# Kernel optimization log

Hardware: AMD Instinct MI355X
Metric: run time of the kernel (lower is better)

## Reference

```python
import jax, jax.numpy as jnp
import numpy as np

B, T, C, H = 4, 2048, 1024, 16
D = C // H  # head dim = 64

def setup_inputs() -> dict:
    key = jax.random.key(0)
    k1, k2, k3 = jax.random.split(key, 3)
    x = jax.random.normal(k1, (B, T, C), dtype=jnp.float32)
    w_attn = jax.random.normal(k2, (C, 3 * C), dtype=jnp.float32) * 0.02
    b_attn = jnp.zeros((3 * C,), dtype=jnp.float32)
    w_proj = jax.random.normal(k3, (C, C), dtype=jnp.float32) * 0.02
    b_proj = jnp.zeros((C,), dtype=jnp.float32)
    return {"x": x, "w_attn": w_attn, "b_attn": b_attn, "w_proj": w_proj, "b_proj": b_proj}

def reference(x, w_attn, b_attn, w_proj, b_proj):
    Bx, Tx, Cx = x.shape
    qkv = x @ w_attn + b_attn  # [B, T, 3C]
    q, k, v = jnp.split(qkv, 3, axis=2)
    # [B, H, T, D]
    q = q.reshape(Bx, Tx, H, D).swapaxes(1, 2)
    k = k.reshape(Bx, Tx, H, D).swapaxes(1, 2)
    v = v.reshape(Bx, Tx, H, D).swapaxes(1, 2)
    scale = 1.0 / jnp.sqrt(jnp.asarray(D, dtype=x.dtype))
    att = jnp.einsum('bhqd,bhkd->bhqk', q, k) * scale  # [B, H, T, T]
    causal = jnp.tril(jnp.ones((Tx, Tx), dtype=bool))
    att = jnp.where(causal[None, None], att, -jnp.inf)
    att = jax.nn.softmax(att, axis=-1)
    y = jnp.einsum('bhqk,bhkd->bhqd', att, v)  # [B, H, T, D]
    y = y.swapaxes(1, 2).reshape(Bx, Tx, Cx)
    return y @ w_proj + b_proj
```

## Files before the change

kernel.cpp:

```cpp
#include <hip/hip_runtime.h>
#include <hip/hip_bf16.h>
#include <cstdint>

#define B_ 4
#define T_ 2048
#define C_ 1024
#define H_ 16
#define D_ 64

#define BM 128
#define BN 128
#define BK 64
#define NT (C_ / BK)

typedef __bf16 bf16x8 __attribute__((ext_vector_type(8)));
typedef float f32x4 __attribute__((ext_vector_type(4)));

static __device__ __forceinline__ unsigned short f2bf(float f) {
    unsigned int i = __float_as_uint(f);
    unsigned int r = (i + 0x7FFFu + ((i >> 16) & 1u)) >> 16;
    return (unsigned short)r;
}
static __device__ __forceinline__ float exp2_fast(float x) {
    float r;
    asm("v_exp_f32 %0, %1" : "=v"(r) : "v"(x));
    return r;
}

static __device__ __forceinline__ void gl_lds16(const unsigned short* g,
                                                unsigned short* l) {
    __builtin_amdgcn_global_load_lds(
        (const __attribute__((address_space(1))) unsigned int*)g,
        (__attribute__((address_space(3))) unsigned int*)l, 16, 0, 0);
}

__global__ __launch_bounds__(256)
void convert_f32_bf16(const float* __restrict__ in,
                      unsigned short* __restrict__ out, int n) {
    int i = (blockIdx.x * 256 + threadIdx.x) * 8;
    if (i < n) {
        float4 a = *(const float4*)(in + i);
        float4 b = *(const float4*)(in + i + 4);
        ushort4 s0 = {f2bf(a.x), f2bf(a.y), f2bf(a.z), f2bf(a.w)};
        ushort4 s1 = {f2bf(b.x), f2bf(b.y), f2bf(b.z), f2bf(b.w)};
        *(ushort4*)(out + i) = s0;
        *(ushort4*)(out + i + 4) = s1;
    }
}

__global__ void transpose_f32_bf16(const float* __restrict__ in,
                                   unsigned short* __restrict__ out,
                                   int R, int Cc) {
    __shared__ unsigned short tile[32][33];
    int c0 = blockIdx.x * 32;
    int r0 = blockIdx.y * 32;
    int tx = threadIdx.x, ty = threadIdx.y;
    #pragma unroll
    for (int i = ty; i < 32; i += 8)
        tile[i][tx] = f2bf(in[(size_t)(r0 + i) * Cc + c0 + tx]);
    __syncthreads();
    #pragma unroll
    for (int i = ty; i < 32; i += 8)
        out[(size_t)(c0 + i) * R + r0 + tx] = tile[tx][i];
}

#define GEMM128_CORE(APTR, ASTRIDE, BTPTR)                                    \
    int tid = threadIdx.x;                                                    \
    int nwg = gridDim.x * gridDim.y;                                          \
    int flat = blockIdx.y * gridDim.x + blockIdx.x;                           \
    int swz = (flat & 7) * (nwg >> 3) + (flat >> 3);                          \
    int bx = swz % gridDim.x;                                                 \
    int by = swz / gridDim.x;                                                 \
    int row0 = by * BM;                                                       \
    int col0 = bx * BN;                                                       \
    int wave = tid >> 6, lane = tid & 63;                                     \
    int wm = wave >> 1, wn = wave & 1;                                        \
    int m16 = lane & 15, quad = lane >> 4;                                    \
    int srow = tid >> 3;                                                      \
    int scs = ((tid & 7) ^ (srow & 7)) * 8;                                   \
    const unsigned short* aps = (APTR) + (size_t)(row0 + srow) * (ASTRIDE)    \
                                + scs;                                        \
    const unsigned short* bps = (BTPTR) + (size_t)(col0 + srow) * C_ + scs;   \
    f32x4 acc[4][4];                                                          \
    _Pragma("unroll")                                                         \
    for (int i = 0; i < 4; ++i)                                               \
    _Pragma("unroll")                                                         \
    for (int j = 0; j < 4; ++j)                                               \
        acc[i][j] = (f32x4){0.f, 0.f, 0.f, 0.f};                              \
    auto STAGE = [&](int t, int buf) {                                        \
        int koff = t * BK;                                                    \
        unsigned short* ad = smem + buf * 8192 + tid * 8;                     \
        unsigned short* bd = smem + 16384 + buf * 8192 + tid * 8;             \
        _Pragma("unroll")                                                     \
        for (int l = 0; l < 4; ++l) {                                         \
            gl_lds16(aps + (size_t)(l * 32) * (ASTRIDE) + koff, ad + l * 2048);\
            gl_lds16(bps + (size_t)(l * 32) * C_ + koff, bd + l * 2048);      \
        }                                                                     \
    };                                                                        \
    int rbA = wm * 64 + m16;                                                  \
    int rbB = wn * 64 + m16;                                                  \
    int pc0 = ((0 + quad) ^ (m16 & 7)) * 8;                                   \
    int pc1 = ((4 + quad) ^ (m16 & 7)) * 8;                                   \
    STAGE(0, 0);                                                              \
    asm volatile("s_waitcnt vmcnt(0)" ::: "memory");                          \
    __builtin_amdgcn_s_barrier();                                             \
    for (int t = 0; t < NT; ++t) {                                            \
        int buf = t & 1;                                                      \
        if (t + 1 < NT) STAGE(t + 1, buf ^ 1);                                \
        const unsigned short* Abuf = smem + buf * 8192;                       \
        const unsigned short* Bbuf = smem + 16384 + buf * 8192;               \
        bf16x8 a0[4], a1[4], b0[4], b1[4];                                    \
        _Pragma("unroll")                                                     \
        for (int i = 0; i < 4; ++i) {                                         \
            a0[i] = *(const bf16x8*)(Abuf + (rbA + i * 16) * 64 + pc0);       \
            a1[i] = *(const bf16x8*)(Abuf + (rbA + i * 16) * 64 + pc1);       \
        }                                                                     \
        _Pragma("unroll")                                                     \
        for (int j = 0; j < 4; ++j) {                                         \
            b0[j] = *(const bf16x8*)(Bbuf + (rbB + j * 16) * 64 + pc0);       \
            b1[j] = *(const bf16x8*)(Bbuf + (rbB + j * 16) * 64 + pc1);       \
        }                                                                     \
        __builtin_amdgcn_s_setprio(1);                                        \
        _Pragma("unroll")                                                     \
        for (int i = 0; i < 4; ++i)                                           \
        _Pragma("unroll")                                                     \
        for (int j = 0; j < 4; ++j) {                                         \
            acc[i][j] = __builtin_amdgcn_mfma_f32_16x16x32_bf16(              \
                a0[i], b0[j], acc[i][j], 0, 0, 0);                            \
            acc[i][j] = __builtin_amdgcn_mfma_f32_16x16x32_bf16(              \
                a1[i], b1[j], acc[i][j], 0, 0, 0);                            \
        }                                                                     \
        __builtin_amdgcn_s_setprio(0);                                        \
        asm volatile("s_waitcnt vmcnt(0)" ::: "memory");                      \
        __builtin_amdgcn_s_barrier();                                        \
    }                                                                         \
    __syncthreads();

__global__ __launch_bounds__(256, 2)
void gemm_qkv(const unsigned short* __restrict__ A,
              const unsigned short* __restrict__ Bt,
              const float* __restrict__ bias,
              unsigned short* __restrict__ qkv,
              unsigned short* __restrict__ vt,
              int M, float qscale) {
    __shared__ __align__(16) unsigned short smem[32768];
    GEMM128_CORE(A, C_, Bt)

    float bv[4];
    #pragma unroll
    for (int j = 0; j < 4; ++j)
        bv[j] = bias[col0 + wn * 64 + j * 16 + m16];

    unsigned short* wbuf = smem + wave * 2048;
    bool isV = (col0 >= 2 * C_);
    float sc = (col0 < C_) ? qscale : 1.0f;
    int b_loc = row0 >> 11;
    int trow0 = (row0 & 2047) + wm * 64;
    int head = isV ? ((col0 - 2 * C_ + wn * 64) >> 6) : 0;
    unsigned short* vtb = vt + (size_t)((b_loc * H_ + head) * 64) * T_;

    #pragma unroll
    for (int sub = 0; sub < 4; ++sub) {
        int i0 = (sub >> 1) << 1;
        int j0 = (sub & 1) << 1;
        #pragma unroll
        for (int jj = 0; jj < 2; ++jj) {
            #pragma unroll
            for (int ii = 0; ii < 2; ++ii) {
                #pragma unroll
                for (int rr = 0; rr < 4; ++rr) {
                    int rl = ii * 16 + quad * 4 + rr;
                    int cl = jj * 16 + m16;
                    unsigned short hv =
                        f2bf((acc[i0 + ii][j0 + jj][rr] + bv[j0 + jj]) * sc);
                    if (!isV) wbuf[rl * 40 + cl] = hv;
                    else      wbuf[cl * 40 + rl] = hv;
                }
            }
        }
        __builtin_amdgcn_sched_barrier(0);
        if (!isV) {
            #pragma unroll
            for (int it = 0; it < 4; ++it) {
                int rl = it * 8 + (lane >> 3);
                int cc = (lane & 7) << 2;
                uint2 v2 = *(const uint2*)&wbuf[rl * 40 + cc];
                int rowg = row0 + wm * 64 + i0 * 16 + rl;
                int colg = col0 + wn * 64 + j0 * 16 + cc;
                *(uint2*)&qkv[(size_t)rowg * (2 * C_) + colg] = v2;
            }
        } else {
            #pragma unroll
            for (int it = 0; it < 4; ++it) {
                int dsub = it * 8 + (lane >> 3);
                int tc = (lane & 7) << 2;
                uint2 v2 = *(const uint2*)&wbuf[dsub * 40 + tc];
                int d = j0 * 16 + dsub;
                int tg = trow0 + i0 * 16 + tc;
                *(uint2*)&vtb[(size_t)d * T_ + tg] = v2;
            }
        }
        __builtin_amdgcn_sched_barrier(0);
    }
}

__global__ __launch_bounds__(256, 2)
void gemm_out(const unsigned short* __restrict__ A,
              const unsigned short* __restrict__ Bt,
              const float* __restrict__ bias,
              float* __restrict__ Cmat,
              int M) {
    const int N = C_;
    __shared__ __align__(16) unsigned short smem[32768];
    GEMM128_CORE(A, (2 * C_), Bt)

    #pragma unroll
    for (int j = 0; j < 4; ++j) {
        int col = col0 + wn * 64 + j * 16 + m16;
        float bvv = bias[col];
        #pragma unroll
        for (int i = 0; i < 4; ++i) {
            int row = row0 + wm * 64 + i * 16 + quad * 4;
            #pragma unroll
            for (int rr = 0; rr < 4; ++rr)
                Cmat[(size_t)(row + rr) * N + col] = acc[i][j][rr] + bvv;
        }
    }
}

__global__ __launch_bounds__(256)
void attn_mfma(unsigned short* __restrict__ qkv,
               const unsigned short* __restrict__ vt) {
    __shared__ __align__(16) unsigned short Ks[2][64][64];
    __shared__ __align__(16) unsigned short Vs[2][64][64];
    __shared__ __align__(16) unsigned short Pb[4][16][72];

    int bh = blockIdx.x;
    int b = bh >> 4, h = bh & 15;
    int qb = (T_ / 64 - 1) - blockIdx.y;
    int tid = threadIdx.x;
    int wave = tid >> 6;
    int lane = tid & 63;
    int m16 = lane & 15, quad = lane >> 4;

    const size_t rs = 2 * C_;
    unsigned short* base = qkv + (size_t)b * T_ * rs + h * 64;
    const unsigned short* kb0 = base + C_;
    const unsigned short* vtb = vt + (size_t)bh * 64 * T_;

    int qrow = qb * 64 + wave * 16 + m16;
    const unsigned short* qp = base + (size_t)qrow * rs;
    bf16x8 qf0 = *(const bf16x8*)(qp + quad * 8);
    bf16x8 qf1 = *(const bf16x8*)(qp + 32 + quad * 8);

    f32x4 o[4];
    #pragma unroll
    for (int dt = 0; dt < 4; ++dt) o[dt] = (f32x4){0.f, 0.f, 0.f, 0.f};
    float lrow[4] = {0.f, 0.f, 0.f, 0.f};

    int qg0 = qb * 64 + wave * 16 + quad * 4;
    int ntiles = qb + 1;

    int srow = tid >> 3;
    int schs = ((tid & 7) ^ (srow & 7)) * 8;
    const unsigned short* kps = kb0 + (size_t)srow * rs + schs;
    const unsigned short* vps = vtb + (size_t)srow * T_ + schs;
    unsigned short* kdst = &Ks[0][0][0] + wave * 512;
    unsigned short* vdst = &Vs[0][0][0] + wave * 512;

    auto STAGE = [&](int kt, int buf) {
        const unsigned short* ks = kps + (size_t)(kt * 64) * rs;
        const unsigned short* vs = vps + kt * 64;
        unsigned short* kd = kdst + buf * 4096;
        unsigned short* vd = vdst + buf * 4096;
        gl_lds16(ks, kd);
        gl_lds16(ks + (size_t)32 * rs, kd + 2048);
        gl_lds16(vs, vd);
        gl_lds16(vs + (size_t)32 * T_, vd + 2048);
    };

    int kpc0 = ((0 + quad) ^ (m16 & 7)) << 3;
    int kpc1 = ((4 + quad) ^ (m16 & 7)) << 3;

    STAGE(0, 0);
    asm volatile("s_waitcnt vmcnt(0)" ::: "memory");
    __builtin_amdgcn_s_barrier();

    for (int kt = 0; kt < ntiles; ++kt) {
        int cur = kt & 1;
        if (kt + 1 < ntiles) STAGE(kt + 1, cur ^ 1);

        f32x4 s[4];
        #pragma unroll
        for (int st = 0; st < 4; ++st) {
            f32x4 acc = (f32x4){0.f, 0.f, 0.f, 0.f};
            bf16x8 k0 = *(const bf16x8*)&Ks[cur][st * 16 + m16][kpc0];
            bf16x8 k1 = *(const bf16x8*)&Ks[cur][st * 16 + m16][kpc1];
            __builtin_amdgcn_s_setprio(1);
            acc = __builtin_amdgcn_mfma_f32_16x16x32_bf16(qf0, k0, acc, 0, 0, 0);
            acc = __builtin_amdgcn_mfma_f32_16x16x32_bf16(qf1, k1, acc, 0, 0, 0);
            __builtin_amdgcn_s_setprio(0);
            s[st] = acc;
        }

        if (kt == qb) {
            #pragma unroll
            for (int st = 0; st < 4; ++st) {
                int kg = kt * 64 + st * 16 + m16;
                #pragma unroll
                for (int r = 0; r < 4; ++r)
                    if (kg > qg0 + r) s[st][r] = -1.0e30f;
            }
        }

        #pragma unroll
        for (int st = 0; st < 4; ++st) {
            #pragma unroll
            for (int r = 0; r < 4; ++r) {
                float p = exp2_fast(s[st][r]);
                lrow[r] += p;
                Pb[wave][quad * 4 + r][st * 16 + m16] = f2bf(p);
            }
        }
        __builtin_amdgcn_sched_barrier(0);

        #pragma unroll
        for (int s2 = 0; s2 < 2; ++s2) {
            bf16x8 pa = *(const bf16x8*)&Pb[wave][m16][s2 * 32 + quad * 8];
            int vpc = ((s2 * 4 + quad) ^ (m16 & 7)) << 3;
            __builtin_amdgcn_s_setprio(1);
            #pragma unroll
            for (int dt = 0; dt < 4; ++dt) {
                bf16x8 vv = *(const bf16x8*)&Vs[cur][dt * 16 + m16][vpc];
                o[dt] = __builtin_amdgcn_mfma_f32_16x16x32_bf16(pa, vv, o[dt], 0, 0, 0);
            }
            __builtin_amdgcn_s_setprio(0);
        }

        asm volatile("s_waitcnt vmcnt(0)" ::: "memory");
        __builtin_amdgcn_s_barrier();
    }

    float lf[4];
    #pragma unroll
    for (int r = 0; r < 4; ++r) lf[r] = lrow[r];
    #pragma unroll
    for (int off = 1; off <= 8; off <<= 1)
        #pragma unroll
        for (int r = 0; r < 4; ++r)
            lf[r] += __shfl_xor(lf[r], off);

    #pragma unroll
    for (int r = 0; r < 4; ++r) {
        float inv = 1.0f / lf[r];
        unsigned short* op = base + (size_t)(qg0 + r) * rs;
        #pragma unroll
        for (int dt = 0; dt < 4; ++dt)
            op[dt * 16 + m16] = f2bf(o[dt][r] * inv);
    }
}

extern "C" void kernel_launch(void* const* d_in, const int* in_sizes, int n_in,
                              void* d_out, int out_size, void* d_ws, size_t ws_size,
                              hipStream_t stream) {
    const float* x      = (const float*)d_in[0];
    const float* w_attn = (const float*)d_in[1];
    const float* b_attn = (const float*)d_in[2];
    const float* w_proj = (const float*)d_in[3];
    const float* b_proj = (const float*)d_in[4];
    float* out = (float*)d_out;

    unsigned short* ws = (unsigned short*)d_ws;
    unsigned short* xb       = ws;
    unsigned short* w_attn_t = xb + (size_t)B_ * T_ * C_;
    unsigned short* w_proj_t = w_attn_t + (size_t)3 * C_ * C_;
    unsigned short* qkv      = w_proj_t + (size_t)C_ * C_;

    const size_t fixed_hw = (size_t)B_ * T_ * C_ + 4 * (size_t)C_ * C_;
    const size_t per_b_hw = (size_t)T_ * 2 * C_ + (size_t)H_ * 64 * T_;
    int bstep = (ws_size >= (fixed_hw + (size_t)B_ * per_b_hw) * sizeof(unsigned short))
                ? B_ : 1;

    int nx = B_ * T_ * C_;
    convert_f32_bf16<<<nx / 2048, 256, 0, stream>>>(x, xb, nx);
    transpose_f32_bf16<<<dim3(3 * C_ / 32, C_ / 32), dim3(32, 8), 0, stream>>>(
        w_attn, w_attn_t, C_, 3 * C_);
    transpose_f32_bf16<<<dim3(C_ / 32, C_ / 32), dim3(32, 8), 0, stream>>>(
        w_proj, w_proj_t, C_, C_);

    const float QSCALE = 0.125f * 1.44269504088896341f;

    for (int b0 = 0; b0 < B_; b0 += bstep) {
        int M = bstep * T_;
        const unsigned short* xbb = xb + (size_t)b0 * T_ * C_;
        unsigned short* vt = qkv + (size_t)bstep * T_ * 2 * C_;

        gemm_qkv<<<dim3(3 * C_ / BN, M / BM), 256, 0, stream>>>(
            xbb, w_attn_t, b_attn, qkv, vt, M, QSCALE);

        attn_mfma<<<dim3(bstep * H_, T_ / 64), 256, 0, stream>>>(qkv, vt);

        gemm_out<<<dim3(C_ / BN, M / BM), 256, 0, stream>>>(
            qkv, w_proj_t, b_proj, out + (size_t)b0 * T_ * C_, M);
    }
}
```

Measured before the change: 256.5 us.

## Double attention query tile to 128 rows per block so K/V loads are reused

```diff
diff --git a/kernel.cpp b/kernel.cpp
--- a/kernel.cpp
+++ b/kernel.cpp
@@ -20,6 +20,12 @@
     unsigned int i = __float_as_uint(f);
     unsigned int r = (i + 0x7FFFu + ((i >> 16) & 1u)) >> 16;
     return (unsigned short)r;
+}
+static __device__ __forceinline__ unsigned short f2bf_hw(float f) {
+    __bf16 h = (__bf16)f;
+    union { __bf16 h; unsigned short u; } cv;
+    cv.h = h;
+    return cv.u;
 }
 static __device__ __forceinline__ float exp2_fast(float x) {
     float r;
@@ -228,16 +234,16 @@
     }
 }
 
-__global__ __launch_bounds__(256)
+__global__ __launch_bounds__(256, 3)
 void attn_mfma(unsigned short* __restrict__ qkv,
                const unsigned short* __restrict__ vt) {
     __shared__ __align__(16) unsigned short Ks[2][64][64];
     __shared__ __align__(16) unsigned short Vs[2][64][64];
-    __shared__ __align__(16) unsigned short Pb[4][16][72];
+    __shared__ __align__(16) unsigned short Pb[4][32][72];
 
     int bh = blockIdx.x;
     int b = bh >> 4, h = bh & 15;
-    int qb = (T_ / 64 - 1) - blockIdx.y;
+    int qb = (T_ / 128 - 1) - blockIdx.y;
     int tid = threadIdx.x;
     int wave = tid >> 6;
     int lane = tid & 63;
@@ -248,18 +254,27 @@
     const unsigned short* kb0 = base + C_;
     const unsigned short* vtb = vt + (size_t)bh * 64 * T_;
 
-    int qrow = qb * 64 + wave * 16 + m16;
-    const unsigned short* qp = base + (size_t)qrow * rs;
-    bf16x8 qf0 = *(const bf16x8*)(qp + quad * 8);
-    bf16x8 qf1 = *(const bf16x8*)(qp + 32 + quad * 8);
-
-    f32x4 o[4];
-    #pragma unroll
-    for (int dt = 0; dt < 4; ++dt) o[dt] = (f32x4){0.f, 0.f, 0.f, 0.f};
-    float lrow[4] = {0.f, 0.f, 0.f, 0.f};
-
-    int qg0 = qb * 64 + wave * 16 + quad * 4;
-    int ntiles = qb + 1;
+    bf16x8 qf0[2], qf1[2];
+    #pragma unroll
+    for (int f = 0; f < 2; ++f) {
+        int qrow = qb * 128 + wave * 32 + f * 16 + m16;
+        const unsigned short* qp = base + (size_t)qrow * rs;
+        qf0[f] = *(const bf16x8*)(qp + quad * 8);
+        qf1[f] = *(const bf16x8*)(qp + 32 + quad * 8);
+    }
+
+    f32x4 o[2][4];
+    #pragma unroll
+    for (int f = 0; f < 2; ++f)
+        #pragma unroll
+        for (int dt = 0; dt < 4; ++dt) o[f][dt] = (f32x4){0.f, 0.f, 0.f, 0.f};
+    float lrow[2][4] = {{0.f, 0.f, 0.f, 0.f}, {0.f, 0.f, 0.f, 0.f}};
+
+    int qg0[2];
+    qg0[0] = qb * 128 + wave * 32 + quad * 4;
+    qg0[1] = qg0[0] + 16;
+
+    int ntiles = 2 * qb + 2;
 
     int srow = tid >> 3;
     int schs = ((tid & 7) ^ (srow & 7)) * 8;
@@ -290,73 +305,86 @@
         int cur = kt & 1;
         if (kt + 1 < ntiles) STAGE(kt + 1, cur ^ 1);
 
-        f32x4 s[4];
+        f32x4 s[2][4];
         #pragma unroll
         for (int st = 0; st < 4; ++st) {
-            f32x4 acc = (f32x4){0.f, 0.f, 0.f, 0.f};
             bf16x8 k0 = *(const bf16x8*)&Ks[cur][st * 16 + m16][kpc0];
             bf16x8 k1 = *(const bf16x8*)&Ks[cur][st * 16 + m16][kpc1];
             __builtin_amdgcn_s_setprio(1);
-            acc = __builtin_amdgcn_mfma_f32_16x16x32_bf16(qf0, k0, acc, 0, 0, 0);
-            acc = __builtin_amdgcn_mfma_f32_16x16x32_bf16(qf1, k1, acc, 0, 0, 0);
-            __builtin_amdgcn_s_setprio(0);
-            s[st] = acc;
-        }
-
-        if (kt == qb) {
-            #pragma unroll
-            for (int st = 0; st < 4; ++st) {
-                int kg = kt * 64 + st * 16 + m16;
-                #pragma unroll
-                for (int r = 0; r < 4; ++r)
-                    if (kg > qg0 + r) s[st][r] = -1.0e30f;
-            }
-        }
-
-        #pragma unroll
-        for (int st = 0; st < 4; ++st) {
-            #pragma unroll
-            for (int r = 0; r < 4; ++r) {
-                float p = exp2_fast(s[st][r]);
-                lrow[r] += p;
-                Pb[wave][quad * 4 + r][st * 16 + m16] = f2bf(p);
-            }
-        }
-        __builtin_amdgcn_sched_barrier(0);
-
-        #pragma unroll
-        for (int s2 = 0; s2 < 2; ++s2) {
-            bf16x8 pa = *(const bf16x8*)&Pb[wave][m16][s2 * 32 + quad * 8];
-            int vpc = ((s2 * 4 + quad) ^ (m16 & 7)) << 3;
-            __builtin_amdgcn_s_setprio(1);
-            #pragma unroll
-            for (int dt = 0; dt < 4; ++dt) {
-                bf16x8 vv = *(const bf16x8*)&Vs[cur][dt * 16 + m16][vpc];
-                o[dt] = __builtin_amdgcn_mfma_f32_16x16x32_bf16(pa, vv, o[dt], 0, 0, 0);
+            #pragma unroll
+            for (int f = 0; f < 2; ++f) {
+                f32x4 a = (f32x4){0.f, 0.f, 0.f, 0.f};
+                a = __builtin_amdgcn_mfma_f32_16x16x32_bf16(qf0[f], k0, a, 0, 0, 0);
+                a = __builtin_amdgcn_mfma_f32_16x16x32_bf16(qf1[f], k1, a, 0, 0, 0);
+                s[f][st] = a;
             }
             __builtin_amdgcn_s_setprio(0);
         }
 
+        if (kt >= 2 * qb) {
+            #pragma unroll
+            for (int f = 0; f < 2; ++f)
+                #pragma unroll
+                for (int st = 0; st < 4; ++st) {
+                    int kg = kt * 64 + st * 16 + m16;
+                    #pragma unroll
+                    for (int r = 0; r < 4; ++r)
+                        if (kg > qg0[f] + r) s[f][st][r] = -1.0e30f;
+                }
+        }
+
+        #pragma unroll
+        for (int f = 0; f < 2; ++f)
+            #pragma unroll
+            for (int st = 0; st < 4; ++st)
+                #pragma unroll
+                for (int r = 0; r < 4; ++r) {
+                    float p = exp2_fast(s[f][st][r]);
+                    lrow[f][r] += p;
+                    Pb[wave][f * 16 + quad * 4 + r][st * 16 + m16] = f2bf_hw(p);
+                }
+        __builtin_amdgcn_sched_barrier(0);
+
+        #pragma unroll
+        for (int s2 = 0; s2 < 2; ++s2) {
+            int vpc = ((s2 * 4 + quad) ^ (m16 & 7)) << 3;
+            #pragma unroll
+            for (int f = 0; f < 2; ++f) {
+                bf16x8 pa = *(const bf16x8*)&Pb[wave][f * 16 + m16][s2 * 32 + quad * 8];
+                __builtin_amdgcn_s_setprio(1);
+                #pragma unroll
+                for (int dt = 0; dt < 4; ++dt) {
+                    bf16x8 vv = *(const bf16x8*)&Vs[cur][dt * 16 + m16][vpc];
+                    o[f][dt] = __builtin_amdgcn_mfma_f32_16x16x32_bf16(
+                        pa, vv, o[f][dt], 0, 0, 0);
+                }
+                __builtin_amdgcn_s_setprio(0);
+            }
+        }
+
         asm volatile("s_waitcnt vmcnt(0)" ::: "memory");
         __builtin_amdgcn_s_barrier();
     }
 
-    float lf[4];
-    #pragma unroll
-    for (int r = 0; r < 4; ++r) lf[r] = lrow[r];
-    #pragma unroll
-    for (int off = 1; off <= 8; off <<= 1)
-        #pragma unroll
-        for (int r = 0; r < 4; ++r)
-            lf[r] += __shfl_xor(lf[r], off);
-
-    #pragma unroll
-    for (int r = 0; r < 4; ++r) {
-        float inv = 1.0f / lf[r];
-        unsigned short* op = base + (size_t)(qg0 + r) * rs;
-        #pragma unroll
-        for (int dt = 0; dt < 4; ++dt)
-            op[dt * 16 + m16] = f2bf(o[dt][r] * inv);
+    #pragma unroll
+    for (int f = 0; f < 2; ++f) {
+        float lf[4];
+        #pragma unroll
+        for (int r = 0; r < 4; ++r) lf[r] = lrow[f][r];
+        #pragma unroll
+        for (int off = 1; off <= 8; off <<= 1)
+            #pragma unroll
+            for (int r = 0; r < 4; ++r)
+                lf[r] += __shfl_xor(lf[r], off);
+
+        #pragma unroll
+        for (int r = 0; r < 4; ++r) {
+            float inv = 1.0f / lf[r];
+            unsigned short* op = base + (size_t)(qg0[f] + r) * rs;
+            #pragma unroll
+            for (int dt = 0; dt < 4; ++dt)
+                op[dt * 16 + m16] = f2bf(o[f][dt][r] * inv);
+        }
     }
 }
 
@@ -398,7 +426,7 @@
         gemm_qkv<<<dim3(3 * C_ / BN, M / BM), 256, 0, stream>>>(
             xbb, w_attn_t, b_attn, qkv, vt, M, QSCALE);
 
-        attn_mfma<<<dim3(bstep * H_, T_ / 64), 256, 0, stream>>>(qkv, vt);
+        attn_mfma<<<dim3(bstep * H_, T_ / 128), 256, 0, stream>>>(qkv, vt);
 
         gemm_out<<<dim3(C_ / BN, M / BM), 256, 0, stream>>>(
             qkv, w_proj_t, b_proj, out + (size_t)b0 * T_ * C_, M);
```

Result: faster. 249.7 us (-2.6%).
